# Performance work log

Measured on AMD Instinct MI355X. Metric: run time of the kernel, lower is better.

The kernel has to match this reference:

```python
import jax, jax.numpy as jnp
import numpy as np
import math

RC = 3.6            # cutoff radius
SMOOTH_W = 0.3      # ShiftedCosine smoothing width
N_RAD = 12          # max_radial=11 -> 12 radial functions
L_MAX = 3           # max_angular
N_TYPES = 3
BOX = 27.4
# neighbor-type pairs a1<=a2 (keys_to_properties layout), sqrt(2) for off-diagonal
PAIR_A1 = np.array([0, 0, 0, 1, 1, 2])
PAIR_A2 = np.array([0, 1, 2, 1, 2, 2])
PAIR_FACT = np.where(PAIR_A1 != PAIR_A2, np.sqrt(2.0), 1.0).astype(np.float32)


def _gto_setup():
    # GTO primitives g_n(r) = N_n r^n exp(-r^2/(2 sigma_n^2)), orthonormalized via S^{-1/2}
    n = np.arange(N_RAD, dtype=np.float64)
    sigma = RC * np.maximum(np.sqrt(n), 1.0) / N_RAD
    gam = np.array([math.gamma(v) for v in (n + 1.5)])
    norm = 1.0 / np.sqrt(0.5 * gam * sigma ** (2 * n + 3))
    npow = n[:, None] + n[None, :]
    c = 0.5 / sigma[:, None] ** 2 + 0.5 / sigma[None, :] ** 2
    gam2 = np.vectorize(math.gamma)((npow + 3.0) / 2.0)
    S = norm[:, None] * norm[None, :] * 0.5 * gam2 * c ** (-(npow + 3.0) / 2.0)
    w, V = np.linalg.eigh(S)
    Sinv_half = (V * (1.0 / np.sqrt(w))) @ V.T
    return sigma.astype(np.float32), norm.astype(np.float32), Sinv_half.astype(np.float32)

SIGMA, NORM, SINV = _gto_setup()


def radial_basis(r):
    # r [...,] -> [..., N_RAD] orthonormalized GTO values
    n = jnp.arange(N_RAD, dtype=r.dtype)
    sig = jnp.asarray(SIGMA)
    g = jnp.asarray(NORM) * r[..., None] ** n * jnp.exp(-0.5 * r[..., None] ** 2 / sig ** 2)
    return g @ jnp.asarray(SINV)


def real_sph_l3(u):
    # real spherical harmonics l=0..3 on unit vectors u [...,3] -> [...,16]
    x, y, z = u[..., 0], u[..., 1], u[..., 2]
    x2, y2, z2 = x * x, y * y, z * z
    one = jnp.ones_like(x)
    return jnp.stack([
        0.28209479177387814 * one,
        0.4886025119029199 * y, 0.4886025119029199 * z, 0.4886025119029199 * x,
        1.0925484305920792 * x * y, 1.0925484305920792 * y * z,
        0.31539156525252005 * (3.0 * z2 - 1.0),
        1.0925484305920792 * x * z, 0.5462742152960396 * (x2 - y2),
        0.5900435899266435 * y * (3.0 * x2 - y2), 2.890611442640554 * x * y * z,
        0.4570457994644658 * y * (5.0 * z2 - 1.0), 0.3731763325901154 * z * (5.0 * z2 - 3.0),
        0.4570457994644658 * x * (5.0 * z2 - 1.0), 1.445305721320277 * z * (x2 - y2),
        0.5900435899266435 * x * (3.0 * x2 - y2),
    ], axis=-1)


def cutoff_fn(r):
    # ShiftedCosine: 1 for r<rc-w, cosine switch on [rc-w, rc], 0 beyond
    t = jnp.clip((r - (RC - SMOOTH_W)) / SMOOTH_W, 0.0, 1.0)
    return 0.5 * (1.0 + jnp.cos(jnp.pi * t))


def soap_features(positions, species):
    B, N, _ = positions.shape
    rvec = positions[:, :, None, :] - positions[:, None, :, :]  # [B,N,N,3]
    d2 = jnp.sum(rvec * rvec, axis=-1)
    nonself = ~jnp.eye(N, dtype=bool)[None]
    dist = jnp.sqrt(jnp.where(nonself, d2, 1.0))                 # safe for grads
    w = cutoff_fn(dist) * nonself                                 # [B,N,N] pair weight
    unit = rvec / dist[..., None]
    R = radial_basis(dist) * w[..., None]                         # [B,N,N,12]
    Y = real_sph_l3(unit)                                         # [B,N,N,16]
    T = jax.nn.one_hot(species, N_TYPES, dtype=positions.dtype)   # [B,N,3]
    # density expansion coefficients c_{i,a,n,lm}
    c = jnp.einsum('bja,bijn,bijk->biank', T, R, Y)               # [B,N,3,12,16]
    c1 = c[:, :, PAIR_A1]                                         # [B,N,6,12,16]
    c2 = c[:, :, PAIR_A2]
    l_slices = [(0, 1), (1, 4), (4, 9), (9, 16)]
    ps = []
    for l, (s, e) in enumerate(l_slices):
        p = jnp.einsum('bipnm,bipqm->bipnq', c1[..., s:e], c2[..., s:e])
        ps.append(p / jnp.sqrt(jnp.asarray(2.0 * l + 1.0, positions.dtype)))
    p = jnp.stack(ps, axis=-1)                                    # [B,N,6,12,12,4]
    p = p * jnp.asarray(PAIR_FACT)[:, None, None, None]
    return p.reshape(B * N, -1)                                   # [B*N, 3456]


def setup_inputs() -> dict:
    key = jax.random.key(0)
    k0, k1, k2 = jax.random.split(key, 3)
    positions = jax.random.uniform(k0, (4, 1024, 3), dtype=jnp.float32) * BOX
    species = jax.random.randint(k1, (4, 1024), 0, N_TYPES, dtype=jnp.int32)
    W = jax.random.normal(k2, (3456,), dtype=jnp.float32) * 0.02
    b = jnp.zeros((1,), dtype=jnp.float32)
    return {"positions": positions, "species": species, "W": W, "b": b}


def reference(positions, species, W, b):
    feats = soap_features(positions, species)   # [B*N, 3456]
    return feats @ W[:, None] + b               # per-atom energies [B*N, 1]
```

## Files before the change

kernel.cpp:

```cpp
#include <hip/hip_runtime.h>
#include <math.h>

#define NRAD   12
#define NSPH   16
#define NTYPE  3
#define NATOM  1024
#define MAXNBR 32
#define RCUT   3.6f
#define APB    4

#define RSTR   12
#define YSTR   16
#define CSTR   20

#define NPAIR  144

#define SQRT2F 1.41421356237309515f
#define LS1    0.57735026918962576f
#define LS2    0.44721359549995794f
#define LS3    0.37796447300922722f

struct SoapConsts {
    float norm[NRAD];
    float inv2sig2[NRAD];
    float sinv[NRAD * NRAD];
};

static void compute_consts(SoapConsts* C) {
    double G[26];
    G[2] = 1.0;
    G[3] = 0.88622692545275801364908374167057259139877;
    for (int t = 4; t < 26; ++t) G[t] = (0.5 * t - 1.0) * G[t - 2];

    double sigma[NRAD], norm[NRAD];
    for (int n = 0; n < NRAD; ++n) {
        double sq = sqrt((double)n);
        if (sq < 1.0) sq = 1.0;
        sigma[n] = 3.6 * sq / 12.0;
        norm[n]  = 1.0 / sqrt(0.5 * G[2 * n + 3] * pow(sigma[n], 2.0 * n + 3.0));
    }

    double S[NRAD][NRAD];
    for (int i = 0; i < NRAD; ++i)
        for (int j = 0; j < NRAD; ++j) {
            double c = 0.5 / (sigma[i] * sigma[i]) + 0.5 / (sigma[j] * sigma[j]);
            double e = 0.5 * (i + j + 3.0);
            S[i][j]  = norm[i] * norm[j] * 0.5 * G[i + j + 3] * pow(c, -e);
        }

    double A[NRAD][NRAD], V[NRAD][NRAD];
    for (int i = 0; i < NRAD; ++i)
        for (int j = 0; j < NRAD; ++j) {
            A[i][j] = S[i][j];
            V[i][j] = (i == j) ? 1.0 : 0.0;
        }
    for (int sweep = 0; sweep < 60; ++sweep) {
        double off = 0.0;
        for (int p = 0; p < NRAD - 1; ++p)
            for (int q = p + 1; q < NRAD; ++q) off += A[p][q] * A[p][q];
        if (off < 1e-26) break;
        for (int p = 0; p < NRAD - 1; ++p) {
            for (int q = p + 1; q < NRAD; ++q) {
                double apq = A[p][q];
                if (fabs(apq) < 1e-300) continue;
                double tau = (A[q][q] - A[p][p]) / (2.0 * apq);
                double tt  = ((tau >= 0.0) ? 1.0 : -1.0) / (fabs(tau) + sqrt(1.0 + tau * tau));
                double cc  = 1.0 / sqrt(1.0 + tt * tt);
                double ss  = tt * cc;
                for (int k = 0; k < NRAD; ++k) {
                    double akp = A[k][p], akq = A[k][q];
                    A[k][p] = cc * akp - ss * akq;
                    A[k][q] = ss * akp + cc * akq;
                }
                for (int k = 0; k < NRAD; ++k) {
                    double apk = A[p][k], aqk = A[q][k];
                    A[p][k] = cc * apk - ss * aqk;
                    A[q][k] = ss * apk + cc * aqk;
                }
                for (int k = 0; k < NRAD; ++k) {
                    double vkp = V[k][p], vkq = V[k][q];
                    V[k][p] = cc * vkp - ss * vkq;
                    V[k][q] = ss * vkp + cc * vkq;
                }
            }
        }
    }
    double wisr[NRAD];
    for (int k = 0; k < NRAD; ++k) wisr[k] = 1.0 / sqrt(A[k][k]);
    for (int i = 0; i < NRAD; ++i)
        for (int j = 0; j < NRAD; ++j) {
            double s = 0.0;
            for (int k = 0; k < NRAD; ++k) s += V[i][k] * wisr[k] * V[j][k];
            C->sinv[i * NRAD + j] = (float)s;
        }
    for (int n = 0; n < NRAD; ++n) {
        C->norm[n]     = (float)norm[n];
        C->inv2sig2[n] = (float)(0.5 / (sigma[n] * sigma[n]));
    }
}

__device__ __forceinline__ void ldrow(const float* __restrict__ row, float* r) {
    const float4* p = reinterpret_cast<const float4*>(row);
    float4 a = p[0], b = p[1], c = p[2], d = p[3];
    r[0]=a.x;  r[1]=a.y;  r[2]=a.z;  r[3]=a.w;
    r[4]=b.x;  r[5]=b.y;  r[6]=b.z;  r[7]=b.w;
    r[8]=c.x;  r[9]=c.y;  r[10]=c.z; r[11]=c.w;
    r[12]=d.x; r[13]=d.y; r[14]=d.z; r[15]=d.w;
}

__device__ __forceinline__ float4 ld4(const float* p) {
    return *reinterpret_cast<const float4*>(p);
}

__device__ __forceinline__ float dot4l(const float* c1, const float* c2,
                                       float4 w4, float fact) {
    float d0 = c1[0]*c2[0];
    float d1 = c1[1]*c2[1] + c1[2]*c2[2] + c1[3]*c2[3];
    float d2 = c1[4]*c2[4] + c1[5]*c2[5] + c1[6]*c2[6] + c1[7]*c2[7]
             + c1[8]*c2[8];
    float d3 = c1[9]*c2[9] + c1[10]*c2[10] + c1[11]*c2[11] + c1[12]*c2[12]
             + c1[13]*c2[13] + c1[14]*c2[14] + c1[15]*c2[15];
    return fact * (w4.x * d0 + (LS1 * w4.y) * d1
                 + (LS2 * w4.z) * d2 + (LS3 * w4.w) * d3);
}

__global__ __launch_bounds__(256, 4) void soap_kernel(
    const float* __restrict__ positions,
    const int*   __restrict__ species,
    const float* __restrict__ W,
    const float* __restrict__ bias,
    float*       __restrict__ out,
    SoapConsts C)
{
    const int wid  = threadIdx.x >> 6;
    const int lane = threadIdx.x & 63;
    const int atom = blockIdx.x * APB + wid;
    const int b    = atom >> 10;
    const int i    = atom & (NATOM - 1);

    __shared__ float pbuf[3][NATOM];
    __shared__ int   nbPk[APB][MAXNBR];
    __shared__ float nbR[APB][MAXNBR][RSTR];
    __shared__ float nbY[APB][MAXNBR][YSTR];
    __shared__ float cbuf[APB][NTYPE][NRAD * CSTR];

    {
        const float4* aos4 = reinterpret_cast<const float4*>(positions + b * NATOM * 3);
        for (int idx = threadIdx.x; idx < NATOM * 3 / 4; idx += 256) {
            float4 v = aos4[idx];
            int f0 = idx * 4;
            #pragma unroll
            for (int c = 0; c < 4; ++c) {
                int f = f0 + c;
                int j = f / 3;
                int comp = f - 3 * j;
                float val = (c == 0) ? v.x : (c == 1) ? v.y : (c == 2) ? v.z : v.w;
                pbuf[comp][j] = val;
            }
        }
    }
    __syncthreads();

    const float xi = pbuf[0][i], yi = pbuf[1][i], zi = pbuf[2][i];

    int nNbr = 0;
    const float rc2 = RCUT * RCUT;
    for (int base = 0; base < NATOM; base += 64) {
        int j = base + lane;
        float dx = xi - pbuf[0][j];
        float dy = yi - pbuf[1][j];
        float dz = zi - pbuf[2][j];
        float d2 = dx * dx + dy * dy + dz * dz;
        bool pred = (j != i) && (d2 < rc2);
        unsigned long long m = __ballot(pred);
        if (pred) {
            int slot = nNbr + __popcll(m & ((1ull << lane) - 1ull));
            if (slot < MAXNBR) nbPk[wid][slot] = j;
        }
        nNbr += __popcll(m);
    }
    if (nNbr > MAXNBR) nNbr = MAXNBR;
    __syncthreads();

    if (lane < nNbr) {
        int j = nbPk[wid][lane];
        float dx = xi - pbuf[0][j];
        float dy = yi - pbuf[1][j];
        float dz = zi - pbuf[2][j];
        float d2 = dx * dx + dy * dy + dz * dz;
        float d  = sqrtf(d2);
        float inv = 1.0f / d;
        float ux = dx * inv, uy = dy * inv, uz = dz * inv;

        float t = (d - (RCUT - 0.3f)) * (1.0f / 0.3f);
        t = fminf(fmaxf(t, 0.0f), 1.0f);
        float w = 0.5f * (1.0f + cosf(3.14159265358979323846f * t));

        float g[NRAD];
        float rp = 1.0f;
        #pragma unroll
        for (int n = 0; n < NRAD; ++n) {
            g[n] = C.norm[n] * rp * expf(-d2 * C.inv2sig2[n]) * w;
            rp *= d;
        }
        #pragma unroll
        for (int mm = 0; mm < NRAD; ++mm) {
            float s = 0.0f;
            #pragma unroll
            for (int n = 0; n < NRAD; ++n) s += g[n] * C.sinv[n * NRAD + mm];
            nbR[wid][lane][mm] = s;
        }

        float x2 = ux * ux, y2 = uy * uy, z2 = uz * uz;
        nbY[wid][lane][0]  = 0.28209479177387814f;
        nbY[wid][lane][1]  = 0.4886025119029199f * uy;
        nbY[wid][lane][2]  = 0.4886025119029199f * uz;
        nbY[wid][lane][3]  = 0.4886025119029199f * ux;
        nbY[wid][lane][4]  = 1.0925484305920792f * ux * uy;
        nbY[wid][lane][5]  = 1.0925484305920792f * uy * uz;
        nbY[wid][lane][6]  = 0.31539156525252005f * (3.0f * z2 - 1.0f);
        nbY[wid][lane][7]  = 1.0925484305920792f * ux * uz;
        nbY[wid][lane][8]  = 0.5462742152960396f * (x2 - y2);
        nbY[wid][lane][9]  = 0.5900435899266435f * uy * (3.0f * x2 - y2);
        nbY[wid][lane][10] = 2.890611442640554f * ux * uy * uz;
        nbY[wid][lane][11] = 0.4570457994644658f * uy * (5.0f * z2 - 1.0f);
        nbY[wid][lane][12] = 0.3731763325901154f * uz * (5.0f * z2 - 3.0f);
        nbY[wid][lane][13] = 0.4570457994644658f * ux * (5.0f * z2 - 1.0f);
        nbY[wid][lane][14] = 1.445305721320277f * uz * (x2 - y2);
        nbY[wid][lane][15] = 0.5900435899266435f * ux * (3.0f * x2 - y2);
        nbPk[wid][lane] = j | (species[b * NATOM + j] << 16);
    }
    __syncthreads();

    float a0[3], a1_[3], a2_[3];
    int mI[3], kI[3];
    #pragma unroll
    for (int t = 0; t < 3; ++t) {
        a0[t] = a1_[t] = a2_[t] = 0.0f;
        int mk = lane + t * 64;
        mI[t] = mk >> 4;
        kI[t] = mk & 15;
    }
    for (int j = 0; j < nNbr; ++j) {
        int sp = nbPk[wid][j] >> 16;
        #pragma unroll
        for (int t = 0; t < 3; ++t) {
            float v = nbR[wid][j][mI[t]] * nbY[wid][j][kI[t]];
            a0[t]  += (sp == 0) ? v : 0.0f;
            a1_[t] += (sp == 1) ? v : 0.0f;
            a2_[t] += (sp == 2) ? v : 0.0f;
        }
    }
    #pragma unroll
    for (int t = 0; t < 3; ++t) {
        cbuf[wid][0][mI[t] * CSTR + kI[t]] = a0[t];
        cbuf[wid][1][mI[t] * CSTR + kI[t]] = a1_[t];
        cbuf[wid][2][mI[t] * CSTR + kI[t]] = a2_[t];
    }
    __syncthreads();

    float partial = 0.0f;
    #pragma unroll 1
    for (int t = 0; t < 3; ++t) {
        int pi  = lane + (t << 6);
        bool act = (pi < NPAIR);
        int piC = act ? pi : 0;
        int n = piC / 12;
        int q = piC - 12 * n;
        const float* wbase = W + n * 48 + q * 4;

        float A_[16], B_[16], Cv[16];
        float acc = 0.0f;
        ldrow(&cbuf[wid][0][n * CSTR], A_);
        ldrow(&cbuf[wid][0][q * CSTR], B_);
        ldrow(&cbuf[wid][2][q * CSTR], Cv);
        acc += dot4l(A_, B_, ld4(wbase + 0 * 576), 1.0f);
        ldrow(&cbuf[wid][1][q * CSTR], B_);
        acc += dot4l(A_, B_, ld4(wbase + 1 * 576), SQRT2F);
        acc += dot4l(A_, Cv, ld4(wbase + 2 * 576), SQRT2F);
        ldrow(&cbuf[wid][1][n * CSTR], A_);
        acc += dot4l(A_, B_, ld4(wbase + 3 * 576), 1.0f);
        acc += dot4l(A_, Cv, ld4(wbase + 4 * 576), SQRT2F);
        ldrow(&cbuf[wid][2][n * CSTR], A_);
        acc += dot4l(A_, Cv, ld4(wbase + 5 * 576), 1.0f);

        partial += act ? acc : 0.0f;
    }

    #pragma unroll
    for (int off = 32; off > 0; off >>= 1)
        partial += __shfl_down(partial, off, 64);
    if (lane == 0) out[atom] = partial + bias[0];
}

extern "C" void kernel_launch(void* const* d_in, const int* in_sizes, int n_in,
                              void* d_out, int out_size, void* d_ws, size_t ws_size,
                              hipStream_t stream) {
    const float* positions = (const float*)d_in[0];
    const int*   species   = (const int*)d_in[1];
    const float* W         = (const float*)d_in[2];
    const float* bias      = (const float*)d_in[3];
    float*       out       = (float*)d_out;

    SoapConsts C;
    compute_consts(&C);

    int nAtoms  = in_sizes[0] / 3;
    int nBlocks = nAtoms / APB;
    soap_kernel<<<nBlocks, 64 * APB, 0, stream>>>(positions, species, W, bias, out, C);
}
```

Before: 72.30 us.

## Drop shared position staging, read positions from global, reuse n-rows in power-spectrum contraction

Removes the per-block staging of all 1024 positions into shared memory (and its barrier) and reads neighbor coordinates straight from global memory, relying on cache. This frees about 12 KB of LDS per block, so launch bounds rise to 5 blocks per CU. The power-spectrum contraction is remapped so 48 lanes each hold three n-rows in registers and loop over 3 q values, cutting redundant LDS row loads but leaving 16 lanes idle. Global AoS reads with stride 3 are uncoalesced, and every wave repeats them.

```diff
diff --git a/kernel.cpp b/kernel.cpp
--- a/kernel.cpp
+++ b/kernel.cpp
@@ -12,8 +12,6 @@
 #define RSTR   12
 #define YSTR   16
 #define CSTR   20
-
-#define NPAIR  144
 
 #define SQRT2F 1.41421356237309515f
 #define LS1    0.57735026918962576f
@@ -124,7 +122,7 @@
                  + (LS2 * w4.z) * d2 + (LS3 * w4.w) * d3);
 }
 
-__global__ __launch_bounds__(256, 4) void soap_kernel(
+__global__ __launch_bounds__(256, 5) void soap_kernel(
     const float* __restrict__ positions,
     const int*   __restrict__ species,
     const float* __restrict__ W,
@@ -138,38 +136,21 @@
     const int b    = atom >> 10;
     const int i    = atom & (NATOM - 1);
 
-    __shared__ float pbuf[3][NATOM];
+    const float* pos = positions + b * NATOM * 3;
+    const float xi = pos[3 * i], yi = pos[3 * i + 1], zi = pos[3 * i + 2];
+
     __shared__ int   nbPk[APB][MAXNBR];
     __shared__ float nbR[APB][MAXNBR][RSTR];
     __shared__ float nbY[APB][MAXNBR][YSTR];
     __shared__ float cbuf[APB][NTYPE][NRAD * CSTR];
 
-    {
-        const float4* aos4 = reinterpret_cast<const float4*>(positions + b * NATOM * 3);
-        for (int idx = threadIdx.x; idx < NATOM * 3 / 4; idx += 256) {
-            float4 v = aos4[idx];
-            int f0 = idx * 4;
-            #pragma unroll
-            for (int c = 0; c < 4; ++c) {
-                int f = f0 + c;
-                int j = f / 3;
-                int comp = f - 3 * j;
-                float val = (c == 0) ? v.x : (c == 1) ? v.y : (c == 2) ? v.z : v.w;
-                pbuf[comp][j] = val;
-            }
-        }
-    }
-    __syncthreads();
-
-    const float xi = pbuf[0][i], yi = pbuf[1][i], zi = pbuf[2][i];
-
     int nNbr = 0;
     const float rc2 = RCUT * RCUT;
     for (int base = 0; base < NATOM; base += 64) {
         int j = base + lane;
-        float dx = xi - pbuf[0][j];
-        float dy = yi - pbuf[1][j];
-        float dz = zi - pbuf[2][j];
+        float dx = xi - pos[3 * j];
+        float dy = yi - pos[3 * j + 1];
+        float dz = zi - pos[3 * j + 2];
         float d2 = dx * dx + dy * dy + dz * dz;
         bool pred = (j != i) && (d2 < rc2);
         unsigned long long m = __ballot(pred);
@@ -184,9 +165,9 @@
 
     if (lane < nNbr) {
         int j = nbPk[wid][lane];
-        float dx = xi - pbuf[0][j];
-        float dy = yi - pbuf[1][j];
-        float dz = zi - pbuf[2][j];
+        float dx = xi - pos[3 * j];
+        float dy = yi - pos[3 * j + 1];
+        float dz = zi - pos[3 * j + 2];
         float d2 = dx * dx + dy * dy + dz * dz;
         float d  = sqrtf(d2);
         float inv = 1.0f / d;
@@ -260,31 +241,34 @@
     __syncthreads();
 
     float partial = 0.0f;
-    #pragma unroll 1
-    for (int t = 0; t < 3; ++t) {
-        int pi  = lane + (t << 6);
-        bool act = (pi < NPAIR);
-        int piC = act ? pi : 0;
-        int n = piC / 12;
-        int q = piC - 12 * n;
-        const float* wbase = W + n * 48 + q * 4;
-
-        float A_[16], B_[16], Cv[16];
-        float acc = 0.0f;
-        ldrow(&cbuf[wid][0][n * CSTR], A_);
-        ldrow(&cbuf[wid][0][q * CSTR], B_);
-        ldrow(&cbuf[wid][2][q * CSTR], Cv);
-        acc += dot4l(A_, B_, ld4(wbase + 0 * 576), 1.0f);
-        ldrow(&cbuf[wid][1][q * CSTR], B_);
-        acc += dot4l(A_, B_, ld4(wbase + 1 * 576), SQRT2F);
-        acc += dot4l(A_, Cv, ld4(wbase + 2 * 576), SQRT2F);
-        ldrow(&cbuf[wid][1][n * CSTR], A_);
-        acc += dot4l(A_, B_, ld4(wbase + 3 * 576), 1.0f);
-        acc += dot4l(A_, Cv, ld4(wbase + 4 * 576), SQRT2F);
-        ldrow(&cbuf[wid][2][n * CSTR], A_);
-        acc += dot4l(A_, Cv, ld4(wbase + 5 * 576), 1.0f);
-
-        partial += act ? acc : 0.0f;
+    {
+        const bool act = (lane < 48);
+        const int  ln  = act ? lane : 0;
+        const int  n   = ln >> 2;
+        const int  qb3 = (ln & 3) * 3;
+
+        float cn0[16], cn1[16], cn2[16], B_[16];
+        ldrow(&cbuf[wid][0][n * CSTR], cn0);
+        ldrow(&cbuf[wid][1][n * CSTR], cn1);
+        ldrow(&cbuf[wid][2][n * CSTR], cn2);
+        const float* wrow = W + n * 48;
+
+        #pragma unroll 1
+        for (int t = 0; t < 3; ++t) {
+            int q = qb3 + t;
+            const float* wbase = wrow + q * 4;
+            float acc = 0.0f;
+            ldrow(&cbuf[wid][0][q * CSTR], B_);
+            acc += dot4l(cn0, B_, ld4(wbase + 0 * 576), 1.0f);
+            ldrow(&cbuf[wid][1][q * CSTR], B_);
+            acc += dot4l(cn0, B_, ld4(wbase + 1 * 576), SQRT2F);
+            acc += dot4l(cn1, B_, ld4(wbase + 3 * 576), 1.0f);
+            ldrow(&cbuf[wid][2][q * CSTR], B_);
+            acc += dot4l(cn0, B_, ld4(wbase + 2 * 576), SQRT2F);
+            acc += dot4l(cn1, B_, ld4(wbase + 4 * 576), SQRT2F);
+            acc += dot4l(cn2, B_, ld4(wbase + 5 * 576), 1.0f);
+            partial += act ? acc : 0.0f;
+        }
     }
 
     #pragma unroll
```

Result: slower. 102.1 us (+41.2%).
